# Optimization experiments

Hardware: AMD Instinct MI355X
Metric: run time of the kernel (lower is better)

Reference implementation:

```python
import jax, jax.numpy as jnp
import numpy as np

INPUT_DIM = 1024
HEAD_DIM = 64
BATCH = 4
SEQ = 2048


def setup_inputs() -> dict:
    key = jax.random.key(0)
    ks = jax.random.split(key, 7)
    scale = 1.0 / np.sqrt(INPUT_DIM)
    x = jax.random.normal(ks[0], (BATCH, SEQ, INPUT_DIM), dtype=jnp.float32)
    Wq = jax.random.uniform(ks[1], (INPUT_DIM, HEAD_DIM), jnp.float32, -scale, scale)
    bq = jax.random.uniform(ks[2], (HEAD_DIM,), jnp.float32, -scale, scale)
    Wk = jax.random.uniform(ks[3], (INPUT_DIM, HEAD_DIM), jnp.float32, -scale, scale)
    bk = jax.random.uniform(ks[4], (HEAD_DIM,), jnp.float32, -scale, scale)
    Wv = jax.random.uniform(ks[5], (INPUT_DIM, HEAD_DIM), jnp.float32, -scale, scale)
    bv = jax.random.uniform(ks[6], (HEAD_DIM,), jnp.float32, -scale, scale)
    return {"x": x, "Wq": Wq, "bq": bq, "Wk": Wk, "bk": bk, "Wv": Wv, "bv": bv}


def reference(x, Wq, bq, Wk, bk, Wv, bv):
    # q,k,v: [B, S, Hd]
    q = jnp.einsum('bsd,dh->bsh', x, Wq) + bq
    k = jnp.einsum('bsd,dh->bsh', x, Wk) + bk
    v = jnp.einsum('bsd,dh->bsh', x, Wv) + bv
    scores = jnp.einsum('bqh,bkh->bqk', q, k)  # [B, S, S]
    S = scores.shape[-1]
    # causal mask: 0 on/below diagonal, -inf above (matches torch triu().T trick)
    causal = jnp.tril(jnp.ones((S, S), dtype=bool))
    scores = jnp.where(causal, scores, -jnp.inf)
    # original divides by sqrt(head_dim) AFTER adding mask (-inf stays -inf)
    scores = scores / jnp.sqrt(jnp.asarray(q.shape[-1], scores.dtype))
    attn = jax.nn.softmax(scores, axis=-1)
    return jnp.einsum('bqk,bkh->bqh', attn, v)
```

## Files before the change

kernel.cpp:

```cpp
#include <hip/hip_runtime.h>

#define SEQ  2048
#define DIM  1024
#define HD   64
#define AW   4

typedef float f32x4  __attribute__((ext_vector_type(4)));
typedef short bf16x8 __attribute__((ext_vector_type(8)));

__device__ __forceinline__ short f2bf(float x) {
    union { float f; unsigned u; } v; v.f = x;
    unsigned r = v.u + 0x7FFFu + ((v.u >> 16) & 1u);
    return (short)(r >> 16);
}
__device__ __forceinline__ short f2bf_fast(float x) {
    union { float f; unsigned u; } v; v.f = x;
    return (short)((v.u + 0x8000u) >> 16);
}

#define MFMA16(a, b, c) __builtin_amdgcn_mfma_f32_16x16x32_bf16((a), (b), (c), 0, 0, 0)

#define QSCALE 0.18033688011f

__global__ __launch_bounds__(256) void wprep_kernel(
    const float* __restrict__ Wq, const float* __restrict__ Wk,
    const float* __restrict__ Wv, short* __restrict__ wfrag)
{
    const int idx = blockIdx.x * 256 + threadIdx.x;
    const int l  = idx & 63;
    const int n  = (idx >> 6) & 3;
    const int ks = (idx >> 8) & 31;
    const int w  = idx >> 13;
    const float* __restrict__ W = (w == 0) ? Wq : (w == 1) ? Wk : Wv;
    bf16x8 v;
#pragma unroll
    for (int j = 0; j < 8; ++j)
        v[j] = f2bf(W[(size_t)(ks * 32 + (l >> 4) * 8 + j) * HD + n * 16 + (l & 15)]);
    *reinterpret_cast<bf16x8*>(wfrag + (size_t)idx * 8) = v;
}

__global__ __launch_bounds__(256) void proj_kernel(
    const float* __restrict__ x, const short* __restrict__ wfrag,
    const float* __restrict__ bq, const float* __restrict__ bk,
    const float* __restrict__ bv,
    short* __restrict__ Qs, short* __restrict__ Kb, short* __restrict__ Vt)
{
    __shared__ __align__(16) char smem[49152 + 2304];

    const int tid  = threadIdx.x;
    const int lane = tid & 63;
    const int w    = tid >> 6;
    const int c    = lane & 15;
    const int g    = lane >> 4;
    const int r0   = blockIdx.x * 16;

    f32x4 acc[3][4] = {};
    for (int ks = w * 8; ks < w * 8 + 8; ++ks) {
        const float* xp = x + (size_t)(r0 + c) * DIM + ks * 32 + g * 8;
        float4 a0 = *reinterpret_cast<const float4*>(xp);
        float4 a1 = *reinterpret_cast<const float4*>(xp + 4);
        float av[8] = {a0.x, a0.y, a0.z, a0.w, a1.x, a1.y, a1.z, a1.w};
        bf16x8 af;
#pragma unroll
        for (int j = 0; j < 8; ++j) af[j] = f2bf_fast(av[j]);
#pragma unroll
        for (int which = 0; which < 3; ++which)
#pragma unroll
            for (int n = 0; n < 4; ++n) {
                bf16x8 bfr = *reinterpret_cast<const bf16x8*>(
                    wfrag + ((size_t)((which * 32 + ks) * 4 + n) * 64 + lane) * 8);
                acc[which][n] = MFMA16(af, bfr, acc[which][n]);
            }
    }

    f32x4* red = (f32x4*)smem;
#pragma unroll
    for (int which = 0; which < 3; ++which)
#pragma unroll
        for (int n = 0; n < 4; ++n)
            red[((which * 4 + n) * 4 + w) * 64 + lane] = acc[which][n];
    __syncthreads();

    if (w < 3) {
        const float* __restrict__ bias = (w == 0) ? bq : (w == 1) ? bk : bv;
        f32x4 sum[4];
#pragma unroll
        for (int n = 0; n < 4; ++n) {
            sum[n] = red[((w * 4 + n) * 4 + 0) * 64 + lane];
#pragma unroll
            for (int s = 1; s < 4; ++s)
                sum[n] += red[((w * 4 + n) * 4 + s) * 64 + lane];
        }
        if (w < 2) {
            short* __restrict__ o = (w == 0) ? Qs : Kb;
            const float sc = (w == 0) ? QSCALE : 1.0f;
#pragma unroll
            for (int n = 0; n < 4; ++n) {
                const float bb = bias[n * 16 + c];
#pragma unroll
                for (int i = 0; i < 4; ++i)
                    o[(size_t)(r0 + g * 4 + i) * HD + n * 16 + c] =
                        f2bf((sum[n][i] + bb) * sc);
            }
        } else {
            short* ts = (short*)(smem + 49152);
#pragma unroll
            for (int n = 0; n < 4; ++n) {
                const float bb = bias[n * 16 + c];
#pragma unroll
                for (int i = 0; i < 4; ++i)
                    ts[(g * 4 + i) * 72 + n * 16 + c] = f2bf(sum[n][i] + bb);
            }
            bf16x8 o0, o1;
#pragma unroll
            for (int e = 0; e < 8; ++e) o0[e] = ts[e * 72 + lane];
#pragma unroll
            for (int e = 0; e < 8; ++e) o1[e] = ts[(8 + e) * 72 + lane];
            const int b  = r0 >> 11;
            const int sb = r0 & (SEQ - 1);
            short* dst = Vt + (((size_t)(b * 64 + lane)) << 11) + sb;
            *reinterpret_cast<bf16x8*>(dst)     = o0;
            *reinterpret_cast<bf16x8*>(dst + 8) = o1;
        }
    }
}

__device__ __forceinline__ void loadK(
    const short* __restrict__ Kb, size_t krow0, int key0, int c, int g,
    bf16x8 (&kf)[4][2])
{
#pragma unroll
    for (int n = 0; n < 4; ++n)
#pragma unroll
        for (int st = 0; st < 2; ++st)
            kf[n][st] = *reinterpret_cast<const bf16x8*>(
                Kb + (krow0 + key0 + n * 16 + c) * HD + st * 32 + g * 8);
}
__device__ __forceinline__ void loadV(
    const short* __restrict__ Vt, int batch, int key0, int c, int g,
    bf16x8 (&vf)[2][4])
{
#pragma unroll
    for (int st = 0; st < 2; ++st)
#pragma unroll
        for (int n = 0; n < 4; ++n)
            vf[st][n] = *reinterpret_cast<const bf16x8*>(
                Vt + (((size_t)(batch * 64 + n * 16 + c)) << 11) + key0 + st * 32 + g * 8);
}

__device__ __forceinline__ void qk16(
    const bf16x8 (&kf)[4][2], bf16x8 q0, bf16x8 q1, f32x4 (&S)[4])
{
#pragma unroll
    for (int n = 0; n < 4; ++n) {
        S[n] = MFMA16(q0, kf[n][0], S[n]);
        S[n] = MFMA16(q1, kf[n][1], S[n]);
    }
}

__device__ __forceinline__ void smax_pv(
    f32x4 (&S)[4], bool diag, int key0, int qbase, int c, int g,
    short* P, const bf16x8 (&vf)[2][4],
    f32x4 (&O)[4], float (&m_i)[4], float (&l_i)[4])
{
    if (diag) {
#pragma unroll
        for (int n = 0; n < 4; ++n)
#pragma unroll
            for (int i = 0; i < 4; ++i)
                if (key0 + n * 16 + c > qbase + g * 4 + i)
                    S[n][i] = -__builtin_inff();
    }
    float mx[4], corr[4], rs[4];
#pragma unroll
    for (int i = 0; i < 4; ++i)
        mx[i] = fmaxf(fmaxf(S[0][i], S[1][i]), fmaxf(S[2][i], S[3][i]));
#pragma unroll
    for (int off = 1; off <= 8; off <<= 1)
#pragma unroll
        for (int i = 0; i < 4; ++i)
            mx[i] = fmaxf(mx[i], __shfl_xor(mx[i], off, 64));
#pragma unroll
    for (int i = 0; i < 4; ++i) {
        const float mn = fmaxf(m_i[i], mx[i]);
        corr[i] = exp2f(m_i[i] - mn);
        m_i[i] = mn;
        rs[i] = 0.f;
    }
#pragma unroll
    for (int n = 0; n < 4; ++n)
#pragma unroll
        for (int i = 0; i < 4; ++i) {
            const float p = exp2f(S[n][i] - m_i[i]);
            S[n][i] = p;
            rs[i] += p;
        }
#pragma unroll
    for (int off = 1; off <= 8; off <<= 1)
#pragma unroll
        for (int i = 0; i < 4; ++i)
            rs[i] += __shfl_xor(rs[i], off, 64);
#pragma unroll
    for (int i = 0; i < 4; ++i) l_i[i] = l_i[i] * corr[i] + rs[i];
#pragma unroll
    for (int n = 0; n < 4; ++n)
#pragma unroll
        for (int i = 0; i < 4; ++i) O[n][i] *= corr[i];
#pragma unroll
    for (int n = 0; n < 4; ++n)
#pragma unroll
        for (int i = 0; i < 4; ++i)
            P[(g * 4 + i) * 72 + n * 16 + c] = f2bf_fast(S[n][i]);
#pragma unroll
    for (int st = 0; st < 2; ++st) {
        bf16x8 pf = *reinterpret_cast<const bf16x8*>(&P[c * 72 + st * 32 + g * 8]);
#pragma unroll
        for (int n = 0; n < 4; ++n)
            O[n] = MFMA16(pf, vf[st][n], O[n]);
    }
}

__global__ __launch_bounds__(256) void attn_fused_kernel(
    const short* __restrict__ Qs, const short* __restrict__ Kb,
    const short* __restrict__ Vt, float* __restrict__ out)
{
    __shared__ float  Ost[AW][2][16][68];
    __shared__ float2 mlst[AW][2][16];
    __shared__ short  Pw[AW][2][16 * 72];

    const int tid  = threadIdx.x;
    const int lane = tid & 63;
    const int w    = tid >> 6;
    const int c    = lane & 15;
    const int g    = lane >> 4;

    const int batch = blockIdx.x >> 6;
    const int p     = blockIdx.x & 63;
    const int qlocA = p;
    const int qlocB = 127 - p;
    const int ntA   = (qlocA >> 2) + 1;
    const int ntB   = (qlocB >> 2) + 1;
    const int qbA   = batch * 128 + qlocA;
    const int qbB   = batch * 128 + qlocB;

    bf16x8 qfA0 = *reinterpret_cast<const bf16x8*>(Qs + (size_t)(qbA * 16 + c) * HD + g * 8);
    bf16x8 qfA1 = *reinterpret_cast<const bf16x8*>(Qs + (size_t)(qbA * 16 + c) * HD + 32 + g * 8);
    bf16x8 qfB0 = *reinterpret_cast<const bf16x8*>(Qs + (size_t)(qbB * 16 + c) * HD + g * 8);
    bf16x8 qfB1 = *reinterpret_cast<const bf16x8*>(Qs + (size_t)(qbB * 16 + c) * HD + 32 + g * 8);

    f32x4 OA[4] = {}, OB[4] = {};
    float mA[4], lA[4], mB[4], lB[4];
#pragma unroll
    for (int i = 0; i < 4; ++i) {
        mA[i] = -__builtin_inff(); lA[i] = 0.f;
        mB[i] = -__builtin_inff(); lB[i] = 0.f;
    }

    short* PA = Pw[w][0];
    short* PB = Pw[w][1];
    const size_t krow0 = (size_t)batch * SEQ;

    for (int t = w; t < ntA; t += AW) {
        bf16x8 kf[4][2];
        bf16x8 vf[2][4];
        loadK(Kb, krow0, t * 64, c, g, kf);
        loadV(Vt, batch, t * 64, c, g, vf);
        f32x4 SA[4] = {}, SB[4] = {};
        qk16(kf, qfA0, qfA1, SA);
        qk16(kf, qfB0, qfB1, SB);
        smax_pv(SA, t == ntA - 1, t * 64, qlocA * 16, c, g, PA, vf, OA, mA, lA);
        smax_pv(SB, false,        t * 64, qlocB * 16, c, g, PB, vf, OB, mB, lB);
    }

    {
        int t2 = ntA + (((w - ntA) % AW) + AW) % AW;
        bf16x8 kf[4][2], kfn[4][2];
        if (t2 < ntB) loadK(Kb, krow0, t2 * 64, c, g, kf);
        for (int t = t2; t < ntB; t += AW) {
            const int tn = (t + AW < ntB) ? t + AW : t;
            loadK(Kb, krow0, tn * 64, c, g, kfn);
            bf16x8 vf[2][4];
            loadV(Vt, batch, t * 64, c, g, vf);
            f32x4 SB[4] = {};
            qk16(kf, qfB0, qfB1, SB);
            smax_pv(SB, t == ntB - 1, t * 64, qlocB * 16, c, g, PB, vf, OB, mB, lB);
#pragma unroll
            for (int n = 0; n < 4; ++n) {
                kf[n][0] = kfn[n][0];
                kf[n][1] = kfn[n][1];
            }
        }
    }

#pragma unroll
    for (int n = 0; n < 4; ++n)
#pragma unroll
        for (int i = 0; i < 4; ++i) {
            Ost[w][0][g * 4 + i][n * 16 + c] = OA[n][i];
            Ost[w][1][g * 4 + i][n * 16 + c] = OB[n][i];
        }
    if (c == 0) {
#pragma unroll
        for (int i = 0; i < 4; ++i) {
            mlst[w][0][g * 4 + i] = make_float2(mA[i], lA[i]);
            mlst[w][1][g * 4 + i] = make_float2(mB[i], lB[i]);
        }
    }
    __syncthreads();

    {
        const int s  = w >> 1;
        const int qb = (w >> 1) ? qbB : qbA;
#pragma unroll
        for (int ri = 0; ri < 8; ++ri) {
            const int row = (w & 1) * 8 + ri;
            float M = -__builtin_inff();
#pragma unroll
            for (int wv = 0; wv < AW; ++wv)
                M = fmaxf(M, mlst[wv][s][row].x);
            float l = 0.f, o = 0.f;
#pragma unroll
            for (int wv = 0; wv < AW; ++wv) {
                const float2 ml = mlst[wv][s][row];
                const float wgt = exp2f(ml.x - M);
                l += wgt * ml.y;
                o += wgt * Ost[wv][s][row][lane];
            }
            out[(size_t)(qb * 16 + row) * HD + lane] = o / l;
        }
    }
}

extern "C" void kernel_launch(void* const* d_in, const int* in_sizes, int n_in,
                              void* d_out, int out_size, void* d_ws, size_t ws_size,
                              hipStream_t stream)
{
    (void)in_sizes; (void)n_in; (void)out_size; (void)ws_size;
    const float* x  = (const float*)d_in[0];
    const float* Wq = (const float*)d_in[1];
    const float* bq = (const float*)d_in[2];
    const float* Wk = (const float*)d_in[3];
    const float* bk = (const float*)d_in[4];
    const float* Wv = (const float*)d_in[5];
    const float* bv = (const float*)d_in[6];
    float* out = (float*)d_out;

    char* ws = (char*)d_ws;
    short* Qs    = (short*)(ws);
    short* Kb    = (short*)(ws + (1u << 20));
    short* Vt    = (short*)(ws + (2u << 20));
    short* wfrag = (short*)(ws + (3u << 20));

    wprep_kernel<<<96, 256, 0, stream>>>(Wq, Wk, Wv, wfrag);
    proj_kernel<<<512, 256, 0, stream>>>(x, wfrag, bq, bk, bv, Qs, Kb, Vt);
    attn_fused_kernel<<<256, 256, 0, stream>>>(Qs, Kb, Vt, out);
}
```

Before: 42.88 us.

## Fuse weight prep, projection and attention into one persistent kernel with grid barriers

Merges the three kernels (weight fragment prep, QKV projection, causal attention) into a single 256-block kernel separated by atomic-counter grid barriers, with a memset to reset the counters. The projection now covers 32 rows per block in two passes instead of 16 rows across 512 blocks. The aim is to remove kernel launch gaps and tail effects between stages. In exchange it relies on all 256 blocks being co-resident, spin-wait barrier latency, and halved projection parallelism.

```diff
diff --git a/kernel.cpp b/kernel.cpp
--- a/kernel.cpp
+++ b/kernel.cpp
@@ -4,6 +4,7 @@
 #define DIM  1024
 #define HD   64
 #define AW   4
+#define NBLK 256
 
 typedef float f32x4  __attribute__((ext_vector_type(4)));
 typedef short bf16x8 __attribute__((ext_vector_type(8)));
@@ -22,311 +23,323 @@
 
 #define QSCALE 0.18033688011f
 
-__global__ __launch_bounds__(256) void wprep_kernel(
-    const float* __restrict__ Wq, const float* __restrict__ Wk,
-    const float* __restrict__ Wv, short* __restrict__ wfrag)
-{
-    const int idx = blockIdx.x * 256 + threadIdx.x;
-    const int l  = idx & 63;
-    const int n  = (idx >> 6) & 3;
-    const int ks = (idx >> 8) & 31;
-    const int w  = idx >> 13;
-    const float* __restrict__ W = (w == 0) ? Wq : (w == 1) ? Wk : Wv;
-    bf16x8 v;
-#pragma unroll
-    for (int j = 0; j < 8; ++j)
-        v[j] = f2bf(W[(size_t)(ks * 32 + (l >> 4) * 8 + j) * HD + n * 16 + (l & 15)]);
-    *reinterpret_cast<bf16x8*>(wfrag + (size_t)idx * 8) = v;
-}
-
-__global__ __launch_bounds__(256) void proj_kernel(
-    const float* __restrict__ x, const short* __restrict__ wfrag,
-    const float* __restrict__ bq, const float* __restrict__ bk,
-    const float* __restrict__ bv,
-    short* __restrict__ Qs, short* __restrict__ Kb, short* __restrict__ Vt)
-{
-    __shared__ __align__(16) char smem[49152 + 2304];
+__device__ __forceinline__ void gbar(unsigned* cnt, int s) {
+    __syncthreads();
+    if (threadIdx.x == 0) {
+        __threadfence();
+        atomicAdd(&cnt[s], 1u);
+        while (__hip_atomic_load(&cnt[s], __ATOMIC_RELAXED,
+                                 __HIP_MEMORY_SCOPE_AGENT) < (unsigned)NBLK)
+            __builtin_amdgcn_s_sleep(8);
+        __threadfence();
+    }
+    __syncthreads();
+}
+
+__device__ __forceinline__ void loadK(
+    const short* __restrict__ Kb, size_t krow0, int key0, int c, int g,
+    bf16x8 (&kf)[4][2])
+{
+#pragma unroll
+    for (int n = 0; n < 4; ++n)
+#pragma unroll
+        for (int st = 0; st < 2; ++st)
+            kf[n][st] = *reinterpret_cast<const bf16x8*>(
+                Kb + (krow0 + key0 + n * 16 + c) * HD + st * 32 + g * 8);
+}
+__device__ __forceinline__ void loadV(
+    const short* __restrict__ Vt, int batch, int key0, int c, int g,
+    bf16x8 (&vf)[2][4])
+{
+#pragma unroll
+    for (int st = 0; st < 2; ++st)
+#pragma unroll
+        for (int n = 0; n < 4; ++n)
+            vf[st][n] = *reinterpret_cast<const bf16x8*>(
+                Vt + (((size_t)(batch * 64 + n * 16 + c)) << 11) + key0 + st * 32 + g * 8);
+}
+__device__ __forceinline__ void qk16(
+    const bf16x8 (&kf)[4][2], bf16x8 q0, bf16x8 q1, f32x4 (&S)[4])
+{
+#pragma unroll
+    for (int n = 0; n < 4; ++n) {
+        S[n] = MFMA16(q0, kf[n][0], S[n]);
+        S[n] = MFMA16(q1, kf[n][1], S[n]);
+    }
+}
+
+__device__ __forceinline__ void smax_pv(
+    f32x4 (&S)[4], bool diag, int key0, int qbase, int c, int g,
+    short* P, const bf16x8 (&vf)[2][4],
+    f32x4 (&O)[4], float (&m_i)[4], float (&l_i)[4])
+{
+    if (diag) {
+#pragma unroll
+        for (int n = 0; n < 4; ++n)
+#pragma unroll
+            for (int i = 0; i < 4; ++i)
+                if (key0 + n * 16 + c > qbase + g * 4 + i)
+                    S[n][i] = -__builtin_inff();
+    }
+    float mx[4], corr[4], rs[4];
+#pragma unroll
+    for (int i = 0; i < 4; ++i)
+        mx[i] = fmaxf(fmaxf(S[0][i], S[1][i]), fmaxf(S[2][i], S[3][i]));
+#pragma unroll
+    for (int off = 1; off <= 8; off <<= 1)
+#pragma unroll
+        for (int i = 0; i < 4; ++i)
+            mx[i] = fmaxf(mx[i], __shfl_xor(mx[i], off, 64));
+#pragma unroll
+    for (int i = 0; i < 4; ++i) {
+        const float mn = fmaxf(m_i[i], mx[i]);
+        corr[i] = exp2f(m_i[i] - mn);
+        m_i[i] = mn;
+        rs[i] = 0.f;
+    }
+#pragma unroll
+    for (int n = 0; n < 4; ++n)
+#pragma unroll
+        for (int i = 0; i < 4; ++i) {
+            const float p = exp2f(S[n][i] - m_i[i]);
+            S[n][i] = p;
+            rs[i] += p;
+        }
+#pragma unroll
+    for (int off = 1; off <= 8; off <<= 1)
+#pragma unroll
+        for (int i = 0; i < 4; ++i)
+            rs[i] += __shfl_xor(rs[i], off, 64);
+#pragma unroll
+    for (int i = 0; i < 4; ++i) l_i[i] = l_i[i] * corr[i] + rs[i];
+#pragma unroll
+    for (int n = 0; n < 4; ++n)
+#pragma unroll
+        for (int i = 0; i < 4; ++i) O[n][i] *= corr[i];
+#pragma unroll
+    for (int n = 0; n < 4; ++n)
+#pragma unroll
+        for (int i = 0; i < 4; ++i)
+            P[(g * 4 + i) * 72 + n * 16 + c] = f2bf_fast(S[n][i]);
+#pragma unroll
+    for (int st = 0; st < 2; ++st) {
+        bf16x8 pf = *reinterpret_cast<const bf16x8*>(&P[c * 72 + st * 32 + g * 8]);
+#pragma unroll
+        for (int n = 0; n < 4; ++n)
+            O[n] = MFMA16(pf, vf[st][n], O[n]);
+    }
+}
+
+__global__ __launch_bounds__(256) void fused_all_kernel(
+    const float* __restrict__ x,
+    const float* __restrict__ Wq, const float* __restrict__ bq,
+    const float* __restrict__ Wk, const float* __restrict__ bk,
+    const float* __restrict__ Wv, const float* __restrict__ bv,
+    float* __restrict__ out,
+    short* __restrict__ Qs, short* __restrict__ Kb, short* __restrict__ Vt,
+    short* __restrict__ wfrag, unsigned* __restrict__ bar)
+{
+    __shared__ __align__(16) char smem[55296];
 
     const int tid  = threadIdx.x;
     const int lane = tid & 63;
     const int w    = tid >> 6;
     const int c    = lane & 15;
     const int g    = lane >> 4;
-    const int r0   = blockIdx.x * 16;
-
-    f32x4 acc[3][4] = {};
-    for (int ks = w * 8; ks < w * 8 + 8; ++ks) {
-        const float* xp = x + (size_t)(r0 + c) * DIM + ks * 32 + g * 8;
-        float4 a0 = *reinterpret_cast<const float4*>(xp);
-        float4 a1 = *reinterpret_cast<const float4*>(xp + 4);
-        float av[8] = {a0.x, a0.y, a0.z, a0.w, a1.x, a1.y, a1.z, a1.w};
-        bf16x8 af;
-#pragma unroll
-        for (int j = 0; j < 8; ++j) af[j] = f2bf_fast(av[j]);
+
+    {
+        const int idx = blockIdx.x * 256 + tid;
+        if (idx < 24576) {
+            const int l  = idx & 63;
+            const int n  = (idx >> 6) & 3;
+            const int ks = (idx >> 8) & 31;
+            const int wv = idx >> 13;
+            const float* __restrict__ W = (wv == 0) ? Wq : (wv == 1) ? Wk : Wv;
+            bf16x8 v;
+#pragma unroll
+            for (int j = 0; j < 8; ++j)
+                v[j] = f2bf(W[(size_t)(ks * 32 + (l >> 4) * 8 + j) * HD + n * 16 + (l & 15)]);
+            *reinterpret_cast<bf16x8*>(wfrag + (size_t)idx * 8) = v;
+        }
+    }
+    gbar(bar, 0);
+
+    for (int sub = 0; sub < 2; ++sub) {
+        const int r0 = blockIdx.x * 32 + sub * 16;
+
+        f32x4 acc[3][4] = {};
+        for (int ks = w * 8; ks < w * 8 + 8; ++ks) {
+            const float* xp = x + (size_t)(r0 + c) * DIM + ks * 32 + g * 8;
+            float4 a0 = *reinterpret_cast<const float4*>(xp);
+            float4 a1 = *reinterpret_cast<const float4*>(xp + 4);
+            float av[8] = {a0.x, a0.y, a0.z, a0.w, a1.x, a1.y, a1.z, a1.w};
+            bf16x8 af;
+#pragma unroll
+            for (int j = 0; j < 8; ++j) af[j] = f2bf_fast(av[j]);
+#pragma unroll
+            for (int which = 0; which < 3; ++which)
+#pragma unroll
+                for (int n = 0; n < 4; ++n) {
+                    bf16x8 bfr = *reinterpret_cast<const bf16x8*>(
+                        wfrag + ((size_t)((which * 32 + ks) * 4 + n) * 64 + lane) * 8);
+                    acc[which][n] = MFMA16(af, bfr, acc[which][n]);
+                }
+        }
+
+        f32x4* red = (f32x4*)smem;
 #pragma unroll
         for (int which = 0; which < 3; ++which)
 #pragma unroll
+            for (int n = 0; n < 4; ++n)
+                red[((which * 4 + n) * 4 + w) * 64 + lane] = acc[which][n];
+        __syncthreads();
+
+        if (w < 3) {
+            const float* __restrict__ bias = (w == 0) ? bq : (w == 1) ? bk : bv;
+            f32x4 sum[4];
+#pragma unroll
             for (int n = 0; n < 4; ++n) {
-                bf16x8 bfr = *reinterpret_cast<const bf16x8*>(
-                    wfrag + ((size_t)((which * 32 + ks) * 4 + n) * 64 + lane) * 8);
-                acc[which][n] = MFMA16(af, bfr, acc[which][n]);
-            }
-    }
-
-    f32x4* red = (f32x4*)smem;
-#pragma unroll
-    for (int which = 0; which < 3; ++which)
+                sum[n] = red[((w * 4 + n) * 4 + 0) * 64 + lane];
+#pragma unroll
+                for (int s = 1; s < 4; ++s)
+                    sum[n] += red[((w * 4 + n) * 4 + s) * 64 + lane];
+            }
+            if (w < 2) {
+                short* __restrict__ o = (w == 0) ? Qs : Kb;
+                const float sc = (w == 0) ? QSCALE : 1.0f;
+#pragma unroll
+                for (int n = 0; n < 4; ++n) {
+                    const float bb = bias[n * 16 + c];
+#pragma unroll
+                    for (int i = 0; i < 4; ++i)
+                        o[(size_t)(r0 + g * 4 + i) * HD + n * 16 + c] =
+                            f2bf((sum[n][i] + bb) * sc);
+                }
+            } else {
+                short* ts = (short*)(smem + 49152);
+#pragma unroll
+                for (int n = 0; n < 4; ++n) {
+                    const float bb = bias[n * 16 + c];
+#pragma unroll
+                    for (int i = 0; i < 4; ++i)
+                        ts[(g * 4 + i) * 72 + n * 16 + c] = f2bf(sum[n][i] + bb);
+                }
+                bf16x8 o0, o1;
+#pragma unroll
+                for (int e = 0; e < 8; ++e) o0[e] = ts[e * 72 + lane];
+#pragma unroll
+                for (int e = 0; e < 8; ++e) o1[e] = ts[(8 + e) * 72 + lane];
+                const int b  = r0 >> 11;
+                const int sb = r0 & (SEQ - 1);
+                short* dst = Vt + (((size_t)(b * 64 + lane)) << 11) + sb;
+                *reinterpret_cast<bf16x8*>(dst)     = o0;
+                *reinterpret_cast<bf16x8*>(dst + 8) = o1;
+            }
+        }
+        __syncthreads();
+    }
+    gbar(bar, 1);
+
+    {
+        float*  Ost  = (float*)smem;
+        float2* mlst = (float2*)(smem + 34816);
+        short*  Pw   = (short*)(smem + 35840);
+
+        const int batch = blockIdx.x >> 6;
+        const int p     = blockIdx.x & 63;
+        const int qlocA = p;
+        const int qlocB = 127 - p;
+        const int ntA   = (qlocA >> 2) + 1;
+        const int ntB   = (qlocB >> 2) + 1;
+        const int qbA   = batch * 128 + qlocA;
+        const int qbB   = batch * 128 + qlocB;
+
+        bf16x8 qfA0 = *reinterpret_cast<const bf16x8*>(Qs + (size_t)(qbA * 16 + c) * HD + g * 8);
+        bf16x8 qfA1 = *reinterpret_cast<const bf16x8*>(Qs + (size_t)(qbA * 16 + c) * HD + 32 + g * 8);
+        bf16x8 qfB0 = *reinterpret_cast<const bf16x8*>(Qs + (size_t)(qbB * 16 + c) * HD + g * 8);
+        bf16x8 qfB1 = *reinterpret_cast<const bf16x8*>(Qs + (size_t)(qbB * 16 + c) * HD + 32 + g * 8);
+
+        f32x4 OA[4] = {}, OB[4] = {};
+        float mA[4], lA[4], mB[4], lB[4];
+#pragma unroll
+        for (int i = 0; i < 4; ++i) {
+            mA[i] = -__builtin_inff(); lA[i] = 0.f;
+            mB[i] = -__builtin_inff(); lB[i] = 0.f;
+        }
+
+        short* PA = Pw + (w * 2 + 0) * (16 * 72);
+        short* PB = Pw + (w * 2 + 1) * (16 * 72);
+        const size_t krow0 = (size_t)batch * SEQ;
+
+        for (int t = w; t < ntA; t += AW) {
+            bf16x8 kf[4][2];
+            bf16x8 vf[2][4];
+            loadK(Kb, krow0, t * 64, c, g, kf);
+            loadV(Vt, batch, t * 64, c, g, vf);
+            f32x4 SA[4] = {}, SB[4] = {};
+            qk16(kf, qfA0, qfA1, SA);
+            qk16(kf, qfB0, qfB1, SB);
+            smax_pv(SA, t == ntA - 1, t * 64, qlocA * 16, c, g, PA, vf, OA, mA, lA);
+            smax_pv(SB, false,        t * 64, qlocB * 16, c, g, PB, vf, OB, mB, lB);
+        }
+
+        {
+            int t2 = ntA + (((w - ntA) % AW) + AW) % AW;
+            bf16x8 kf[4][2], kfn[4][2];
+            if (t2 < ntB) loadK(Kb, krow0, t2 * 64, c, g, kf);
+            for (int t = t2; t < ntB; t += AW) {
+                const int tn = (t + AW < ntB) ? t + AW : t;
+                loadK(Kb, krow0, tn * 64, c, g, kfn);
+                bf16x8 vf[2][4];
+                loadV(Vt, batch, t * 64, c, g, vf);
+                f32x4 SB[4] = {};
+                qk16(kf, qfB0, qfB1, SB);
+                smax_pv(SB, t == ntB - 1, t * 64, qlocB * 16, c, g, PB, vf, OB, mB, lB);
+#pragma unroll
+                for (int n = 0; n < 4; ++n) {
+                    kf[n][0] = kfn[n][0];
+                    kf[n][1] = kfn[n][1];
+                }
+            }
+        }
+
+        __syncthreads();
 #pragma unroll
         for (int n = 0; n < 4; ++n)
-            red[((which * 4 + n) * 4 + w) * 64 + lane] = acc[which][n];
-    __syncthreads();
-
-    if (w < 3) {
-        const float* __restrict__ bias = (w == 0) ? bq : (w == 1) ? bk : bv;
-        f32x4 sum[4];
-#pragma unroll
-        for (int n = 0; n < 4; ++n) {
-            sum[n] = red[((w * 4 + n) * 4 + 0) * 64 + lane];
-#pragma unroll
-            for (int s = 1; s < 4; ++s)
-                sum[n] += red[((w * 4 + n) * 4 + s) * 64 + lane];
-        }
-        if (w < 2) {
-            short* __restrict__ o = (w == 0) ? Qs : Kb;
-            const float sc = (w == 0) ? QSCALE : 1.0f;
-#pragma unroll
-            for (int n = 0; n < 4; ++n) {
-                const float bb = bias[n * 16 + c];
-#pragma unroll
-                for (int i = 0; i < 4; ++i)
-                    o[(size_t)(r0 + g * 4 + i) * HD + n * 16 + c] =
-                        f2bf((sum[n][i] + bb) * sc);
-            }
-        } else {
-            short* ts = (short*)(smem + 49152);
-#pragma unroll
-            for (int n = 0; n < 4; ++n) {
-                const float bb = bias[n * 16 + c];
-#pragma unroll
-                for (int i = 0; i < 4; ++i)
-                    ts[(g * 4 + i) * 72 + n * 16 + c] = f2bf(sum[n][i] + bb);
-            }
-            bf16x8 o0, o1;
-#pragma unroll
-            for (int e = 0; e < 8; ++e) o0[e] = ts[e * 72 + lane];
-#pragma unroll
-            for (int e = 0; e < 8; ++e) o1[e] = ts[(8 + e) * 72 + lane];
-            const int b  = r0 >> 11;
-            const int sb = r0 & (SEQ - 1);
-            short* dst = Vt + (((size_t)(b * 64 + lane)) << 11) + sb;
-            *reinterpret_cast<bf16x8*>(dst)     = o0;
-            *reinterpret_cast<bf16x8*>(dst + 8) = o1;
-        }
-    }
-}
-
-__device__ __forceinline__ void loadK(
-    const short* __restrict__ Kb, size_t krow0, int key0, int c, int g,
-    bf16x8 (&kf)[4][2])
-{
-#pragma unroll
-    for (int n = 0; n < 4; ++n)
-#pragma unroll
-        for (int st = 0; st < 2; ++st)
-            kf[n][st] = *reinterpret_cast<const bf16x8*>(
-                Kb + (krow0 + key0 + n * 16 + c) * HD + st * 32 + g * 8);
-}
-__device__ __forceinline__ void loadV(
-    const short* __restrict__ Vt, int batch, int key0, int c, int g,
-    bf16x8 (&vf)[2][4])
-{
-#pragma unroll
-    for (int st = 0; st < 2; ++st)
-#pragma unroll
-        for (int n = 0; n < 4; ++n)
-            vf[st][n] = *reinterpret_cast<const bf16x8*>(
-                Vt + (((size_t)(batch * 64 + n * 16 + c)) << 11) + key0 + st * 32 + g * 8);
-}
-
-__device__ __forceinline__ void qk16(
-    const bf16x8 (&kf)[4][2], bf16x8 q0, bf16x8 q1, f32x4 (&S)[4])
-{
-#pragma unroll
-    for (int n = 0; n < 4; ++n) {
-        S[n] = MFMA16(q0, kf[n][0], S[n]);
-        S[n] = MFMA16(q1, kf[n][1], S[n]);
-    }
-}
-
-__device__ __forceinline__ void smax_pv(
-    f32x4 (&S)[4], bool diag, int key0, int qbase, int c, int g,
-    short* P, const bf16x8 (&vf)[2][4],
-    f32x4 (&O)[4], float (&m_i)[4], float (&l_i)[4])
-{
-    if (diag) {
-#pragma unroll
-        for (int n = 0; n < 4; ++n)
-#pragma unroll
-            for (int i = 0; i < 4; ++i)
-                if (key0 + n * 16 + c > qbase + g * 4 + i)
-                    S[n][i] = -__builtin_inff();
-    }
-    float mx[4], corr[4], rs[4];
-#pragma unroll
-    for (int i = 0; i < 4; ++i)
-        mx[i] = fmaxf(fmaxf(S[0][i], S[1][i]), fmaxf(S[2][i], S[3][i]));
-#pragma unroll
-    for (int off = 1; off <= 8; off <<= 1)
-#pragma unroll
-        for (int i = 0; i < 4; ++i)
-            mx[i] = fmaxf(mx[i], __shfl_xor(mx[i], off, 64));
-#pragma unroll
-    for (int i = 0; i < 4; ++i) {
-        const float mn = fmaxf(m_i[i], mx[i]);
-        corr[i] = exp2f(m_i[i] - mn);
-        m_i[i] = mn;
-        rs[i] = 0.f;
-    }
-#pragma unroll
-    for (int n = 0; n < 4; ++n)
-#pragma unroll
-        for (int i = 0; i < 4; ++i) {
-            const float p = exp2f(S[n][i] - m_i[i]);
-            S[n][i] = p;
-            rs[i] += p;
-        }
-#pragma unroll
-    for (int off = 1; off <= 8; off <<= 1)
-#pragma unroll
-        for (int i = 0; i < 4; ++i)
-            rs[i] += __shfl_xor(rs[i], off, 64);
-#pragma unroll
-    for (int i = 0; i < 4; ++i) l_i[i] = l_i[i] * corr[i] + rs[i];
-#pragma unroll
-    for (int n = 0; n < 4; ++n)
-#pragma unroll
-        for (int i = 0; i < 4; ++i) O[n][i] *= corr[i];
-#pragma unroll
-    for (int n = 0; n < 4; ++n)
-#pragma unroll
-        for (int i = 0; i < 4; ++i)
-            P[(g * 4 + i) * 72 + n * 16 + c] = f2bf_fast(S[n][i]);
-#pragma unroll
-    for (int st = 0; st < 2; ++st) {
-        bf16x8 pf = *reinterpret_cast<const bf16x8*>(&P[c * 72 + st * 32 + g * 8]);
-#pragma unroll
-        for (int n = 0; n < 4; ++n)
-            O[n] = MFMA16(pf, vf[st][n], O[n]);
-    }
-}
-
-__global__ __launch_bounds__(256) void attn_fused_kernel(
-    const short* __restrict__ Qs, const short* __restrict__ Kb,
-    const short* __restrict__ Vt, float* __restrict__ out)
-{
-    __shared__ float  Ost[AW][2][16][68];
-    __shared__ float2 mlst[AW][2][16];
-    __shared__ short  Pw[AW][2][16 * 72];
-
-    const int tid  = threadIdx.x;
-    const int lane = tid & 63;
-    const int w    = tid >> 6;
-    const int c    = lane & 15;
-    const int g    = lane >> 4;
-
-    const int batch = blockIdx.x >> 6;
-    const int p     = blockIdx.x & 63;
-    const int qlocA = p;
-    const int qlocB = 127 - p;
-    const int ntA   = (qlocA >> 2) + 1;
-    const int ntB   = (qlocB >> 2) + 1;
-    const int qbA   = batch * 128 + qlocA;
-    const int qbB   = batch * 128 + qlocB;
-
-    bf16x8 qfA0 = *reinterpret_cast<const bf16x8*>(Qs + (size_t)(qbA * 16 + c) * HD + g * 8);
-    bf16x8 qfA1 = *reinterpret_cast<const bf16x8*>(Qs + (size_t)(qbA * 16 + c) * HD + 32 + g * 8);
-    bf16x8 qfB0 = *reinterpret_cast<const bf16x8*>(Qs + (size_t)(qbB * 16 + c) * HD + g * 8);
-    bf16x8 qfB1 = *reinterpret_cast<const bf16x8*>(Qs + (size_t)(qbB * 16 + c) * HD + 32 + g * 8);
-
-    f32x4 OA[4] = {}, OB[4] = {};
-    float mA[4], lA[4], mB[4], lB[4];
-#pragma unroll
-    for (int i = 0; i < 4; ++i) {
-        mA[i] = -__builtin_inff(); lA[i] = 0.f;
-        mB[i] = -__builtin_inff(); lB[i] = 0.f;
-    }
-
-    short* PA = Pw[w][0];
-    short* PB = Pw[w][1];
-    const size_t krow0 = (size_t)batch * SEQ;
-
-    for (int t = w; t < ntA; t += AW) {
-        bf16x8 kf[4][2];
-        bf16x8 vf[2][4];
-        loadK(Kb, krow0, t * 64, c, g, kf);
-        loadV(Vt, batch, t * 64, c, g, vf);
-        f32x4 SA[4] = {}, SB[4] = {};
-        qk16(kf, qfA0, qfA1, SA);
-        qk16(kf, qfB0, qfB1, SB);
-        smax_pv(SA, t == ntA - 1, t * 64, qlocA * 16, c, g, PA, vf, OA, mA, lA);
-        smax_pv(SB, false,        t * 64, qlocB * 16, c, g, PB, vf, OB, mB, lB);
-    }
-
-    {
-        int t2 = ntA + (((w - ntA) % AW) + AW) % AW;
-        bf16x8 kf[4][2], kfn[4][2];
-        if (t2 < ntB) loadK(Kb, krow0, t2 * 64, c, g, kf);
-        for (int t = t2; t < ntB; t += AW) {
-            const int tn = (t + AW < ntB) ? t + AW : t;
-            loadK(Kb, krow0, tn * 64, c, g, kfn);
-            bf16x8 vf[2][4];
-            loadV(Vt, batch, t * 64, c, g, vf);
-            f32x4 SB[4] = {};
-            qk16(kf, qfB0, qfB1, SB);
-            smax_pv(SB, t == ntB - 1, t * 64, qlocB * 16, c, g, PB, vf, OB, mB, lB);
-#pragma unroll
-            for (int n = 0; n < 4; ++n) {
-                kf[n][0] = kfn[n][0];
-                kf[n][1] = kfn[n][1];
-            }
-        }
-    }
-
-#pragma unroll
-    for (int n = 0; n < 4; ++n)
-#pragma unroll
-        for (int i = 0; i < 4; ++i) {
-            Ost[w][0][g * 4 + i][n * 16 + c] = OA[n][i];
-            Ost[w][1][g * 4 + i][n * 16 + c] = OB[n][i];
-        }
-    if (c == 0) {
-#pragma unroll
-        for (int i = 0; i < 4; ++i) {
-            mlst[w][0][g * 4 + i] = make_float2(mA[i], lA[i]);
-            mlst[w][1][g * 4 + i] = make_float2(mB[i], lB[i]);
-        }
-    }
-    __syncthreads();
-
-    {
-        const int s  = w >> 1;
-        const int qb = (w >> 1) ? qbB : qbA;
-#pragma unroll
-        for (int ri = 0; ri < 8; ++ri) {
-            const int row = (w & 1) * 8 + ri;
-            float M = -__builtin_inff();
-#pragma unroll
-            for (int wv = 0; wv < AW; ++wv)
-                M = fmaxf(M, mlst[wv][s][row].x);
-            float l = 0.f, o = 0.f;
-#pragma unroll
-            for (int wv = 0; wv < AW; ++wv) {
-                const float2 ml = mlst[wv][s][row];
-                const float wgt = exp2f(ml.x - M);
-                l += wgt * ml.y;
-                o += wgt * Ost[wv][s][row][lane];
-            }
-            out[(size_t)(qb * 16 + row) * HD + lane] = o / l;
+#pragma unroll
+            for (int i = 0; i < 4; ++i) {
+                Ost[((w * 2 + 0) * 16 + g * 4 + i) * 68 + n * 16 + c] = OA[n][i];
+                Ost[((w * 2 + 1) * 16 + g * 4 + i) * 68 + n * 16 + c] = OB[n][i];
+            }
+        if (c == 0) {
+#pragma unroll
+            for (int i = 0; i < 4; ++i) {
+                mlst[(w * 2 + 0) * 16 + g * 4 + i] = make_float2(mA[i], lA[i]);
+                mlst[(w * 2 + 1) * 16 + g * 4 + i] = make_float2(mB[i], lB[i]);
+            }
+        }
+        __syncthreads();
+
+        {
+            const int s  = w >> 1;
+            const int qb = (w >> 1) ? qbB : qbA;
+#pragma unroll
+            for (int ri = 0; ri < 8; ++ri) {
+                const int row = (w & 1) * 8 + ri;
+                float M = -__builtin_inff();
+#pragma unroll
+                for (int wv = 0; wv < AW; ++wv)
+                    M = fmaxf(M, mlst[(wv * 2 + s) * 16 + row].x);
+                float l = 0.f, o = 0.f;
+#pragma unroll
+                for (int wv = 0; wv < AW; ++wv) {
+                    const float2 ml = mlst[(wv * 2 + s) * 16 + row];
+                    const float wgt = exp2f(ml.x - M);
+                    l += wgt * ml.y;
+                    o += wgt * Ost[((wv * 2 + s) * 16 + row) * 68 + lane];
+                }
+                out[(size_t)(qb * 16 + row) * HD + lane] = o / l;
+            }
         }
     }
 }
@@ -346,12 +359,13 @@
     float* out = (float*)d_out;
 
     char* ws = (char*)d_ws;
-    short* Qs    = (short*)(ws);
-    short* Kb    = (short*)(ws + (1u << 20));
-    short* Vt    = (short*)(ws + (2u << 20));
-    short* wfrag = (short*)(ws + (3u << 20));
-
-    wprep_kernel<<<96, 256, 0, stream>>>(Wq, Wk, Wv, wfrag);
-    proj_kernel<<<512, 256, 0, stream>>>(x, wfrag, bq, bk, bv, Qs, Kb, Vt);
-    attn_fused_kernel<<<256, 256, 0, stream>>>(Qs, Kb, Vt, out);
-}
+    short*    Qs    = (short*)(ws);
+    short*    Kb    = (short*)(ws + (1u << 20));
+    short*    Vt    = (short*)(ws + (2u << 20));
+    short*    wfrag = (short*)(ws + (3u << 20));
+    unsigned* bar   = (unsigned*)(ws + (1u << 22));
+
+    hipMemsetAsync(bar, 0, 16, stream);
+    fused_all_kernel<<<NBLK, 256, 0, stream>>>(
+        x, Wq, bq, Wk, bk, Wv, bv, out, Qs, Kb, Vt, wfrag, bar);
+}
```

Result: slower. 117.4 us (+173.8%).
